# Kernel tuning notes

Hardware: AMD Instinct MI355X
Metric: run time of the kernel (lower is better)

The kernel has to match this reference:

```python
import jax, jax.numpy as jnp
import numpy as np


def _lstm_layer(x, h0, c0, w_ih, w_hh, b):
    """x: [T,B,I], h0/c0: [B,H], w_ih: [4H,I], w_hh: [4H,H], b: [4H]. PyTorch gate order i,f,g,o."""
    H = h0.shape[-1]
    # Precompute input projection for all timesteps in one big GEMM.
    xg = jnp.einsum('tbi,gi->tbg', x, w_ih) + b  # [T,B,4H]

    def step(carry, xg_t):
        h, c = carry
        g = xg_t + h @ w_hh.T  # [B,4H]
        i, f, gg, o = jnp.split(g, 4, axis=-1)
        c_new = jax.nn.sigmoid(f) * c + jax.nn.sigmoid(i) * jnp.tanh(gg)
        h_new = jax.nn.sigmoid(o) * jnp.tanh(c_new)
        return (h_new, c_new), h_new

    (_, _), hs = jax.lax.scan(step, (h0, c0), xg)
    return hs  # [T,B,H]


def setup_inputs() -> dict:
    key = jax.random.key(0)
    ks = jax.random.split(key, 12)
    T, B, I, H, O, L = 2048, 32, 256, 512, 1024, 2
    s = 1.0 / np.sqrt(H)  # PyTorch LSTM init scale
    return {
        'x': jax.random.normal(ks[0], (T, B, I), jnp.float32),
        'h0': jnp.zeros((L, B, H), jnp.float32),
        'c0': jnp.zeros((L, B, H), jnp.float32),
        'w_ih0': jax.random.normal(ks[1], (4 * H, I), jnp.float32) * s,
        'w_hh0': jax.random.normal(ks[2], (4 * H, H), jnp.float32) * s,
        'b_ih0': jax.random.normal(ks[3], (4 * H,), jnp.float32) * s,
        'b_hh0': jax.random.normal(ks[4], (4 * H,), jnp.float32) * s,
        'w_ih1': jax.random.normal(ks[5], (4 * H, H), jnp.float32) * s,
        'w_hh1': jax.random.normal(ks[6], (4 * H, H), jnp.float32) * s,
        'b_ih1': jax.random.normal(ks[7], (4 * H,), jnp.float32) * s,
        'b_hh1': jax.random.normal(ks[8], (4 * H,), jnp.float32) * s,
        'fc_w': jax.random.normal(ks[9], (O, H), jnp.float32) * s,
        'fc_b': jax.random.normal(ks[10], (O,), jnp.float32) * s,
    }


def reference(x, h0, c0, w_ih0, w_hh0, b_ih0, b_hh0, w_ih1, w_hh1, b_ih1, b_hh1, fc_w, fc_b):
    h1 = _lstm_layer(x, h0[0], c0[0], w_ih0, w_hh0, b_ih0 + b_hh0)   # [T,B,H]
    h2 = _lstm_layer(h1, h0[1], c0[1], w_ih1, w_hh1, b_ih1 + b_hh1)  # [T,B,H]
    logits = h2[-1] @ fc_w.T + fc_b  # out[-1] -> fc, [B,O]
    return jax.nn.log_softmax(logits, axis=1)
```

## Files before the change

### kernel.cpp

```cpp
#include <hip/hip_runtime.h>
#include <stdint.h>

#define TT 2048
#define BB 32
#define II 256
#define HH 512
#define OO 1024
#define NWGL 64
#define NWG 128
#define RING 32
#define SLOTB (BB * HH * 2)

typedef __attribute__((ext_vector_type(8))) short short8;
typedef __attribute__((ext_vector_type(4))) float floatx4;

__device__ __forceinline__ unsigned short f2bf(float f) {
  union { float f; unsigned u; } v; v.f = f;
  unsigned r = v.u + 0x7FFFu + ((v.u >> 16) & 1u);
  return (unsigned short)(r >> 16);
}
__device__ __forceinline__ float bf2f(unsigned short b) {
  union { float f; unsigned u; } v; v.u = ((unsigned)b) << 16; return v.f;
}
__device__ __forceinline__ float sigmf(float x) { return 1.0f / (1.0f + __expf(-x)); }
__device__ __forceinline__ float tanhfast(float x) {
  float xc = fminf(fmaxf(x, -15.f), 15.f);
  float e = __expf(2.f * xc);
  return (e - 1.f) / (e + 1.f);
}

#define LD1(d, va, IMM)                                                     \
  asm volatile("global_load_dwordx4 %0, %1, off offset:" IMM " sc0 sc1"     \
               : "=v"(d) : "v"(va) : "memory")
#define LD1C(d, va, IMM)                                                    \
  asm volatile("global_load_dwordx4 %0, %1, off offset:" IMM                \
               : "=v"(d) : "v"(va) : "memory")

#define ISSUE8(dst, va) do {                                                \
    LD1(dst[0], va, "0");   LD1(dst[1], va, "64");                          \
    LD1(dst[2], va, "128"); LD1(dst[3], va, "192");                         \
    LD1(dst[4], va, "256"); LD1(dst[5], va, "320");                         \
    LD1(dst[6], va, "384"); LD1(dst[7], va, "448"); } while (0)
#define ISSUE8C(dst, va) do {                                               \
    LD1C(dst[0], va, "0");   LD1C(dst[1], va, "64");                        \
    LD1C(dst[2], va, "128"); LD1C(dst[3], va, "192");                       \
    LD1C(dst[4], va, "256"); LD1C(dst[5], va, "320");                       \
    LD1C(dst[6], va, "384"); LD1C(dst[7], va, "448"); } while (0)

#define WAITV(N) do {                                                       \
    asm volatile("s_waitcnt vmcnt(" #N ")" ::: "memory");                   \
    __builtin_amdgcn_sched_barrier(0); } while (0)

#define MF8(tt_, src, wbase) do {                                           \
    _Pragma("unroll")                                                       \
    for (int j = 0; j < 8; j++) {                                           \
      acc[0][tt_] = __builtin_amdgcn_mfma_f32_16x16x32_bf16(src[j], wf[0][(wbase) + j], acc[0][tt_], 0, 0, 0); \
      acc[1][tt_] = __builtin_amdgcn_mfma_f32_16x16x32_bf16(src[j], wf[1][(wbase) + j], acc[1][tt_], 0, 0, 0); \
    } } while (0)

#define PROGREAD(dst, addr64)                                               \
  asm volatile("global_load_dword %0, %1, off sc0 sc1"                      \
               : "=v"(dst) : "v"(addr64) : "memory")

#define SEQSTORE(arr, slot, val) do {                                       \
    if (lane == 0) {                                                        \
      unsigned long long _a = (unsigned long long)(arr) +                   \
          (unsigned long long)((slot) * 64 + g) * 4;                        \
      int _v = (val);                                                       \
      asm volatile("global_store_dword %0, %1, off sc0 sc1"                 \
                   :: "v"(_a), "v"(_v) : "memory");                         \
    } } while (0)

#define TAIL(hwaddr) do {                                                   \
  _Pragma("unroll")                                                         \
  for (int tau = 0; tau < 2; tau++) {                                       \
    _Pragma("unroll")                                                       \
    for (int tt = 0; tt < 2; tt++) {                                        \
      _Pragma("unroll")                                                     \
      for (int r = 0; r < 4; r++) {                                         \
        float val = acc[tau][tt][r];                                        \
        float nl = (gate == 2) ? tanhfast(val) : sigmf(val);                \
        int base2 = (lane & 48) | u;                                        \
        float iv = __shfl(nl, base2);                                       \
        float fv = __shfl(nl, base2 | 4);                                   \
        float gv = __shfl(nl, base2 | 8);                                   \
        float ov = __shfl(nl, base2 | 12);                                  \
        if (gate == 0) {                                                    \
          float cn = fv * cst[tau][tt][r] + iv * gv;                        \
          cst[tau][tt][r] = cn;                                             \
          float hn = ov * tanhfast(cn);                                     \
          int b = tt * 16 + krow * 4 + r;                                   \
          sh[b][tau * 4 + u] = f2bf(hn);                                    \
        }                                                                   \
      }                                                                     \
    }                                                                       \
  }                                                                         \
  asm volatile("s_waitcnt lgkmcnt(0)" ::: "memory");                        \
  __builtin_amdgcn_sched_barrier(0);                                        \
  if (lane < 32) {                                                          \
    short8 v = *reinterpret_cast<const short8*>(&sh[lane][0]);              \
    unsigned long long sa = (hwaddr) + stoff;                               \
    asm volatile("global_store_dwordx4 %0, %1, off sc0 sc1"                 \
                 :: "v"(sa), "v"(v) : "memory");                            \
  } } while (0)

__global__ void k_convert_x(const float* __restrict__ x, ushort* __restrict__ xb, int n4) {
  int i = blockIdx.x * blockDim.x + threadIdx.x;
  int stride = gridDim.x * blockDim.x;
  const float4* xf = reinterpret_cast<const float4*>(x);
  ushort4* ob = reinterpret_cast<ushort4*>(xb);
  for (; i < n4; i += stride) {
    float4 f = xf[i];
    ushort4 o;
    o.x = f2bf(f.x); o.y = f2bf(f.y); o.z = f2bf(f.z); o.w = f2bf(f.w);
    ob[i] = o;
  }
}

__global__ void k_init(const float* __restrict__ h0in,
                       ushort* __restrict__ h0ring, ushort* __restrict__ h1ring,
                       int* __restrict__ h0seq, int* __restrict__ h1seq,
                       int* __restrict__ pr1) {
  int i = threadIdx.x;
  ushort* s0 = h0ring + (RING - 1) * BB * HH;
  ushort* s1 = h1ring + (RING - 1) * BB * HH;
  for (int k = i; k < BB * HH; k += blockDim.x) {
    s0[k] = f2bf(h0in[k]);
    s1[k] = f2bf(h0in[BB * HH + k]);
  }
  for (int k = i; k < RING * 64; k += blockDim.x) {
    int v = (k >= (RING - 1) * 64) ? -1 : (int)0x80000000;
    h0seq[k] = v;
    h1seq[k] = v;
  }
  for (int k = i; k < 64; k += blockDim.x) pr1[k] = -1;
}

__global__ __launch_bounds__(64, 1) void k_lstm(
    const ushort* __restrict__ xb,
    const float* __restrict__ w_ih0, const float* __restrict__ w_hh0,
    const float* __restrict__ b_ih0, const float* __restrict__ b_hh0,
    const float* __restrict__ w_ih1, const float* __restrict__ w_hh1,
    const float* __restrict__ b_ih1, const float* __restrict__ b_hh1,
    const float* __restrict__ c0in,
    ushort* __restrict__ h0ring, ushort* __restrict__ h1ring,
    int* __restrict__ h0seq, int* __restrict__ h1seq,
    int* __restrict__ pr1)
{
  __shared__ ushort sh[BB][8];
  const int wg = blockIdx.x;
  const int lane = threadIdx.x;
  const bool isL0 = wg < NWGL;
  const int g = isL0 ? wg : wg - NWGL;
  const int col = lane & 15;
  const int krow = lane >> 4;
  const int u = col & 3;
  const int gate = col >> 2;

  short8 wf[2][32];
#define LOADW(dst, base, rowlen, kbase, tau) do {                             \
    const int _grow = gate * HH + g * 8 + (tau) * 4 + u;                      \
    const float* _p = (base) + (size_t)_grow * (rowlen) + (kbase) + krow * 8; \
    short8 _r;                                                                \
    _Pragma("unroll")                                                         \
    for (int _j = 0; _j < 8; _j++) _r[_j] = (short)f2bf(_p[_j]);              \
    (dst) = _r; } while (0)

  if (isL0) {
#pragma unroll
    for (int tau = 0; tau < 2; tau++) {
#pragma unroll
      for (int kk = 0; kk < 8; kk++)  LOADW(wf[tau][kk],      w_ih0, II, kk * 32, tau);
#pragma unroll
      for (int kk = 0; kk < 16; kk++) LOADW(wf[tau][8 + kk],  w_hh0, HH, kk * 32, tau);
    }
  } else {
#pragma unroll
    for (int tau = 0; tau < 2; tau++) {
#pragma unroll
      for (int kk = 0; kk < 16; kk++) LOADW(wf[tau][kk],      w_ih1, HH, kk * 32, tau);
#pragma unroll
      for (int kk = 0; kk < 16; kk++) LOADW(wf[tau][16 + kk], w_hh1, HH, kk * 32, tau);
    }
  }
  float bias[2];
#pragma unroll
  for (int tau = 0; tau < 2; tau++) {
    const int grow = gate * HH + g * 8 + tau * 4 + u;
    bias[tau] = isL0 ? (b_ih0[grow] + b_hh0[grow]) : (b_ih1[grow] + b_hh1[grow]);
  }

  float cst[2][2][4];
  {
    const float* cbase = c0in + (isL0 ? 0 : 1) * BB * HH;
#pragma unroll
    for (int tau = 0; tau < 2; tau++)
#pragma unroll
      for (int tt = 0; tt < 2; tt++)
#pragma unroll
        for (int r = 0; r < 4; r++) {
          int b = tt * 16 + krow * 4 + r;
          cst[tau][tt][r] = cbase[b * HH + g * 8 + tau * 4 + u];
        }
  }

  const unsigned long long h0rb = (unsigned long long)h0ring;
  const unsigned long long h1rb = (unsigned long long)h1ring;
  const int vo00 = col * 1024 + krow * 16;
  const unsigned long long stoff = (unsigned long long)(lane * 1024 + g * 16);

  short8 wa[8], wb[8], wc[8], wd[8];
  floatx4 acc[2][2];
  const floatx4 bi0 = (floatx4){ bias[0], bias[0], bias[0], bias[0] };
  const floatx4 bi1 = (floatx4){ bias[1], bias[1], bias[1], bias[1] };

  if (isL0) {
    const unsigned long long xbase = (unsigned long long)xb + (col * 512 + krow * 16);
    for (int t = 0; t < TT; ++t) {
      {
        const unsigned long long sa = (unsigned long long)h0seq +
            (unsigned long long)(((t + 31) & 31) * 64 + lane) * 4;
        int sv; PROGREAD(sv, sa); WAITV(0);
        while (!__all(sv == t - 1)) {
          __builtin_amdgcn_s_sleep(1); PROGREAD(sv, sa); WAITV(0);
        }
      }
      if (((t & 7) == 0) && t >= 32) {
        const unsigned long long pa = (unsigned long long)pr1 + lane * 4ull;
        int pv; PROGREAD(pv, pa); WAITV(0);
        while (!__all(pv >= t - 24)) {
          __builtin_amdgcn_s_sleep(4); PROGREAD(pv, pa); WAITV(0);
        }
      }
      acc[0][0] = bi0; acc[0][1] = bi0; acc[1][0] = bi1; acc[1][1] = bi1;
      const unsigned long long ha = h0rb + (unsigned long long)((t + 31) & 31) * SLOTB + vo00;
      const unsigned long long xa = xbase + (unsigned long long)t * (BB * II * 2);
      ISSUE8(wa, ha); ISSUE8(wb, ha + 512); ISSUE8(wc, ha + 16384); ISSUE8(wd, ha + 16896);
      WAITV(24); MF8(0, wa, 8);  ISSUE8C(wa, xa);
      WAITV(24); MF8(0, wb, 16); ISSUE8C(wb, xa + 8192);
      WAITV(24); MF8(1, wc, 8);
      WAITV(16); MF8(1, wd, 16);
      WAITV(8);  MF8(0, wa, 0);
      WAITV(0);  MF8(1, wb, 0);
      TAIL(h0rb + (unsigned long long)(t & 31) * SLOTB);
      WAITV(0);
      SEQSTORE(h0seq, (t & 31), t);
    }
  } else {
    for (int t = 0; t < TT; ++t) {
      {
        const unsigned long long sa0 = (unsigned long long)h0seq +
            (unsigned long long)((t & 31) * 64 + lane) * 4;
        const unsigned long long sa1 = (unsigned long long)h1seq +
            (unsigned long long)(((t + 31) & 31) * 64 + lane) * 4;
        int s0, s1; PROGREAD(s0, sa0); PROGREAD(s1, sa1); WAITV(0);
        while (!(__all(s0 == t) & __all(s1 == t - 1))) {
          __builtin_amdgcn_s_sleep(1);
          PROGREAD(s0, sa0); PROGREAD(s1, sa1); WAITV(0);
        }
      }
      acc[0][0] = bi0; acc[0][1] = bi0; acc[1][0] = bi1; acc[1][1] = bi1;
      const unsigned long long a0 = h0rb + (unsigned long long)(t & 31) * SLOTB + vo00;
      const unsigned long long a1 = h1rb + (unsigned long long)((t + 31) & 31) * SLOTB + vo00;
      ISSUE8(wa, a0); ISSUE8(wb, a0 + 512); ISSUE8(wc, a0 + 16384); ISSUE8(wd, a0 + 16896);
      WAITV(24); MF8(0, wa, 0); ISSUE8(wa, a1);
      WAITV(24); MF8(0, wb, 8); ISSUE8(wb, a1 + 512);
      WAITV(24); MF8(1, wc, 0); ISSUE8(wc, a1 + 16384);
      WAITV(24); MF8(1, wd, 8); ISSUE8(wd, a1 + 16896);
      WAITV(24); MF8(0, wa, 16);
      WAITV(16); MF8(0, wb, 24);
      WAITV(8);  MF8(1, wc, 16);
      WAITV(0);  MF8(1, wd, 24);
      if (lane == 0) {
        unsigned long long pa = (unsigned long long)pr1 + (unsigned long long)g * 4;
        int pv = t;
        asm volatile("global_store_dword %0, %1, off sc0 sc1"
                     :: "v"(pa), "v"(pv) : "memory");
      }
      TAIL(h1rb + (unsigned long long)(t & 31) * SLOTB);
      WAITV(0);
      SEQSTORE(h1seq, (t & 31), t);
    }
  }
}

__global__ __launch_bounds__(256) void k_fc(const ushort* __restrict__ h1,
                                            const float* __restrict__ fcw,
                                            const float* __restrict__ fcb,
                                            float* __restrict__ out) {
  __shared__ float hsh[HH];
  __shared__ float red[256];
  const int b = blockIdx.x, tid = threadIdx.x;
  for (int k = tid; k < HH; k += 256) hsh[k] = bf2f(h1[b * HH + k]);
  __syncthreads();
  float lg[4];
#pragma unroll
  for (int q = 0; q < 4; q++) {
    int o = q * 256 + tid;
    float acc = fcb[o];
    const float* wr = fcw + (size_t)o * HH;
#pragma unroll 4
    for (int k = 0; k < HH; k += 4) {
      float4 w4 = *reinterpret_cast<const float4*>(wr + k);
      acc += hsh[k] * w4.x + hsh[k + 1] * w4.y + hsh[k + 2] * w4.z + hsh[k + 3] * w4.w;
    }
    lg[q] = acc;
  }
  float m = fmaxf(fmaxf(lg[0], lg[1]), fmaxf(lg[2], lg[3]));
  red[tid] = m; __syncthreads();
  for (int s = 128; s > 0; s >>= 1) { if (tid < s) red[tid] = fmaxf(red[tid], red[tid + s]); __syncthreads(); }
  m = red[0]; __syncthreads();
  float se = 0.f;
#pragma unroll
  for (int q = 0; q < 4; q++) se += __expf(lg[q] - m);
  red[tid] = se; __syncthreads();
  for (int s = 128; s > 0; s >>= 1) { if (tid < s) red[tid] += red[tid + s]; __syncthreads(); }
  float lse = m + logf(red[0]);
#pragma unroll
  for (int q = 0; q < 4; q++) out[b * OO + q * 256 + tid] = lg[q] - lse;
}

extern "C" void kernel_launch(void* const* d_in, const int* in_sizes, int n_in,
                              void* d_out, int out_size, void* d_ws, size_t ws_size,
                              hipStream_t stream) {
  const float* x     = (const float*)d_in[0];
  const float* h0    = (const float*)d_in[1];
  const float* c0    = (const float*)d_in[2];
  const float* w_ih0 = (const float*)d_in[3];
  const float* w_hh0 = (const float*)d_in[4];
  const float* b_ih0 = (const float*)d_in[5];
  const float* b_hh0 = (const float*)d_in[6];
  const float* w_ih1 = (const float*)d_in[7];
  const float* w_hh1 = (const float*)d_in[8];
  const float* b_ih1 = (const float*)d_in[9];
  const float* b_hh1 = (const float*)d_in[10];
  const float* fcw   = (const float*)d_in[11];
  const float* fcb   = (const float*)d_in[12];
  float* out = (float*)d_out;

  char* ws = (char*)d_ws;
  size_t off = 0;
  ushort* xb     = (ushort*)(ws + off); off += (size_t)TT * BB * II * 2;
  ushort* h0ring = (ushort*)(ws + off); off += (size_t)RING * BB * HH * 2;
  ushort* h1ring = (ushort*)(ws + off); off += (size_t)RING * BB * HH * 2;
  int* h0seq = (int*)(ws + off); off += RING * 64 * sizeof(int);
  int* h1seq = (int*)(ws + off); off += RING * 64 * sizeof(int);
  int* pr1   = (int*)(ws + off); off += 64 * sizeof(int);

  k_convert_x<<<2048, 256, 0, stream>>>(x, xb, TT * BB * II / 4);
  k_init<<<1, 256, 0, stream>>>(h0, h0ring, h1ring, h0seq, h1seq, pr1);
  k_lstm<<<NWG, 64, 0, stream>>>(xb, w_ih0, w_hh0, b_ih0, b_hh0,
                                 w_ih1, w_hh1, b_ih1, b_hh1, c0,
                                 h0ring, h1ring, h0seq, h1seq, pr1);
  k_fc<<<BB, 256, 0, stream>>>(h1ring + (RING - 1) * BB * HH, fcw, fcb, out);
}
```

Baseline: 16.87 ms.

## Pack four waves per workgroup and share hidden-state tiles through LDS

Each workgroup now holds four wavefronts instead of one, so there are 32 persistent workgroups instead of 128. Within a workgroup the four waves load the previous hidden state cooperatively into swizzled LDS tiles and then each wave reads its MFMA A operands from LDS. Previously every wave fetched the full hidden state from global memory on its own. Only wave 0 polls the sequence flags, and block barriers order the staging. This cuts global traffic and the number of pollers, but adds two __syncthreads per step on the serial recurrence path and reads x directly with plain loads, which no longer overlap with the h loads.

```diff
diff --git a/kernel.cpp b/kernel.cpp
--- a/kernel.cpp
+++ b/kernel.cpp
@@ -6,8 +6,8 @@
 #define II 256
 #define HH 512
 #define OO 1024
-#define NWGL 64
-#define NWG 128
+#define NWGL 16
+#define NWG 32
 #define RING 32
 #define SLOTB (BB * HH * 2)
 
@@ -32,31 +32,26 @@
 #define LD1(d, va, IMM)                                                     \
   asm volatile("global_load_dwordx4 %0, %1, off offset:" IMM " sc0 sc1"     \
                : "=v"(d) : "v"(va) : "memory")
-#define LD1C(d, va, IMM)                                                    \
-  asm volatile("global_load_dwordx4 %0, %1, off offset:" IMM                \
-               : "=v"(d) : "v"(va) : "memory")
-
-#define ISSUE8(dst, va) do {                                                \
-    LD1(dst[0], va, "0");   LD1(dst[1], va, "64");                          \
-    LD1(dst[2], va, "128"); LD1(dst[3], va, "192");                         \
-    LD1(dst[4], va, "256"); LD1(dst[5], va, "320");                         \
-    LD1(dst[6], va, "384"); LD1(dst[7], va, "448"); } while (0)
-#define ISSUE8C(dst, va) do {                                               \
-    LD1C(dst[0], va, "0");   LD1C(dst[1], va, "64");                        \
-    LD1C(dst[2], va, "128"); LD1C(dst[3], va, "192");                       \
-    LD1C(dst[4], va, "256"); LD1C(dst[5], va, "320");                       \
-    LD1C(dst[6], va, "384"); LD1C(dst[7], va, "448"); } while (0)
+
+#define ISSUE8KB(dst, va) do {                                              \
+    unsigned long long _v1 = (va), _v2 = (va) + 4096;                       \
+    LD1(dst[0], _v1, "0");    LD1(dst[1], _v1, "1024");                     \
+    LD1(dst[2], _v1, "2048"); LD1(dst[3], _v1, "3072");                     \
+    LD1(dst[4], _v2, "0");    LD1(dst[5], _v2, "1024");                     \
+    LD1(dst[6], _v2, "2048"); LD1(dst[7], _v2, "3072"); } while (0)
 
 #define WAITV(N) do {                                                       \
     asm volatile("s_waitcnt vmcnt(" #N ")" ::: "memory");                   \
     __builtin_amdgcn_sched_barrier(0); } while (0)
 
-#define MF8(tt_, src, wbase) do {                                           \
+#define DSW8(buf, tile, w8) do {                                            \
     _Pragma("unroll")                                                       \
-    for (int j = 0; j < 8; j++) {                                           \
-      acc[0][tt_] = __builtin_amdgcn_mfma_f32_16x16x32_bf16(src[j], wf[0][(wbase) + j], acc[0][tt_], 0, 0, 0); \
-      acc[1][tt_] = __builtin_amdgcn_mfma_f32_16x16x32_bf16(src[j], wf[1][(wbase) + j], acc[1][tt_], 0, 0, 0); \
-    } } while (0)
+    for (int j = 0; j < 8; j++)                                             \
+      *reinterpret_cast<short8*>(&(tile)[((w8) + j) * 512 + (lane ^ j) * 8]) = (buf)[j]; \
+    } while (0)
+
+#define LDSA(tile, b, kk)                                                   \
+  (*reinterpret_cast<const short8*>(&(tile)[(b) * 512 + (((kk) * 4 + krow) ^ c7) * 8]))
 
 #define PROGREAD(dst, addr64)                                               \
   asm volatile("global_load_dword %0, %1, off sc0 sc1"                      \
@@ -69,6 +64,14 @@
       int _v = (val);                                                       \
       asm volatile("global_store_dword %0, %1, off sc0 sc1"                 \
                    :: "v"(_a), "v"(_v) : "memory");                         \
+    } } while (0)
+
+#define VALIDATE(arr, slot, tag) do {                                       \
+    const unsigned long long _sa = (unsigned long long)(arr) +              \
+        (unsigned long long)((slot) * 64 + lane) * 4;                       \
+    int _sv; PROGREAD(_sv, _sa); WAITV(0);                                  \
+    while (!__all(_sv == (tag))) {                                          \
+      __builtin_amdgcn_s_sleep(1); PROGREAD(_sv, _sa); WAITV(0);            \
     } } while (0)
 
 #define TAIL(hwaddr) do {                                                   \
@@ -90,7 +93,7 @@
           cst[tau][tt][r] = cn;                                             \
           float hn = ov * tanhfast(cn);                                     \
           int b = tt * 16 + krow * 4 + r;                                   \
-          sh[b][tau * 4 + u] = f2bf(hn);                                    \
+          sh[w][b][tau * 4 + u] = f2bf(hn);                                 \
         }                                                                   \
       }                                                                     \
     }                                                                       \
@@ -98,7 +101,7 @@
   asm volatile("s_waitcnt lgkmcnt(0)" ::: "memory");                        \
   __builtin_amdgcn_sched_barrier(0);                                        \
   if (lane < 32) {                                                          \
-    short8 v = *reinterpret_cast<const short8*>(&sh[lane][0]);              \
+    short8 v = *reinterpret_cast<const short8*>(&sh[w][lane][0]);           \
     unsigned long long sa = (hwaddr) + stoff;                               \
     asm volatile("global_store_dwordx4 %0, %1, off sc0 sc1"                 \
                  :: "v"(sa), "v"(v) : "memory");                            \
@@ -136,7 +139,7 @@
   for (int k = i; k < 64; k += blockDim.x) pr1[k] = -1;
 }
 
-__global__ __launch_bounds__(64, 1) void k_lstm(
+__global__ __launch_bounds__(256, 1) void k_lstm(
     const ushort* __restrict__ xb,
     const float* __restrict__ w_ih0, const float* __restrict__ w_hh0,
     const float* __restrict__ b_ih0, const float* __restrict__ b_hh0,
@@ -147,15 +150,21 @@
     int* __restrict__ h0seq, int* __restrict__ h1seq,
     int* __restrict__ pr1)
 {
-  __shared__ ushort sh[BB][8];
+  __shared__ ushort t0[32 * 512];
+  __shared__ ushort t1[32 * 512];
+  __shared__ ushort sh[4][BB][8];
   const int wg = blockIdx.x;
-  const int lane = threadIdx.x;
+  const int tid = threadIdx.x;
+  const int w = tid >> 6;
+  const int lane = tid & 63;
   const bool isL0 = wg < NWGL;
-  const int g = isL0 ? wg : wg - NWGL;
+  const int G = isL0 ? wg : wg - NWGL;
+  const int g = G * 4 + w;
   const int col = lane & 15;
   const int krow = lane >> 4;
   const int u = col & 3;
   const int gate = col >> 2;
+  const int c7 = col & 7;
 
   short8 wf[2][32];
 #define LOADW(dst, base, rowlen, kbase, tau) do {                             \
@@ -206,49 +215,56 @@
 
   const unsigned long long h0rb = (unsigned long long)h0ring;
   const unsigned long long h1rb = (unsigned long long)h1ring;
-  const int vo00 = col * 1024 + krow * 16;
   const unsigned long long stoff = (unsigned long long)(lane * 1024 + g * 16);
-
-  short8 wa[8], wb[8], wc[8], wd[8];
+  const unsigned long long stagevo = (unsigned long long)(w * 8192 + lane * 16);
+
+  short8 wa[8], wb[8];
   floatx4 acc[2][2];
   const floatx4 bi0 = (floatx4){ bias[0], bias[0], bias[0], bias[0] };
   const floatx4 bi1 = (floatx4){ bias[1], bias[1], bias[1], bias[1] };
 
   if (isL0) {
-    const unsigned long long xbase = (unsigned long long)xb + (col * 512 + krow * 16);
     for (int t = 0; t < TT; ++t) {
-      {
-        const unsigned long long sa = (unsigned long long)h0seq +
-            (unsigned long long)(((t + 31) & 31) * 64 + lane) * 4;
-        int sv; PROGREAD(sv, sa); WAITV(0);
-        while (!__all(sv == t - 1)) {
-          __builtin_amdgcn_s_sleep(1); PROGREAD(sv, sa); WAITV(0);
-        }
-      }
-      if (((t & 7) == 0) && t >= 32) {
-        const unsigned long long pa = (unsigned long long)pr1 + lane * 4ull;
-        int pv; PROGREAD(pv, pa); WAITV(0);
-        while (!__all(pv >= t - 24)) {
-          __builtin_amdgcn_s_sleep(4); PROGREAD(pv, pa); WAITV(0);
-        }
-      }
+      if (w == 0) {
+        VALIDATE(h0seq, (t + 31) & 31, t - 1);
+        if (((t & 7) == 0) && t >= 32) {
+          const unsigned long long pa = (unsigned long long)pr1 + lane * 4ull;
+          int pv; PROGREAD(pv, pa); WAITV(0);
+          while (!__all(pv >= t - 24)) {
+            __builtin_amdgcn_s_sleep(4); PROGREAD(pv, pa); WAITV(0);
+          }
+        }
+      }
+      __syncthreads();
+      ISSUE8KB(wa, h0rb + (unsigned long long)((t + 31) & 31) * SLOTB + stagevo);
+      WAITV(0);
+      DSW8(wa, t0, w * 8);
+      __syncthreads();
       acc[0][0] = bi0; acc[0][1] = bi0; acc[1][0] = bi1; acc[1][1] = bi1;
-      const unsigned long long ha = h0rb + (unsigned long long)((t + 31) & 31) * SLOTB + vo00;
-      const unsigned long long xa = xbase + (unsigned long long)t * (BB * II * 2);
-      ISSUE8(wa, ha); ISSUE8(wb, ha + 512); ISSUE8(wc, ha + 16384); ISSUE8(wd, ha + 16896);
-      WAITV(24); MF8(0, wa, 8);  ISSUE8C(wa, xa);
-      WAITV(24); MF8(0, wb, 16); ISSUE8C(wb, xa + 8192);
-      WAITV(24); MF8(1, wc, 8);
-      WAITV(16); MF8(1, wd, 16);
-      WAITV(8);  MF8(0, wa, 0);
-      WAITV(0);  MF8(1, wb, 0);
+      const char* xr = (const char*)xb + (size_t)t * (BB * II * 2);
+#pragma unroll
+      for (int tt = 0; tt < 2; tt++) {
+        const int b = tt * 16 + col;
+#pragma unroll
+        for (int kk = 0; kk < 8; kk++) {
+          short8 a = *reinterpret_cast<const short8*>(xr + b * 512 + kk * 64 + krow * 16);
+          acc[0][tt] = __builtin_amdgcn_mfma_f32_16x16x32_bf16(a, wf[0][kk], acc[0][tt], 0, 0, 0);
+          acc[1][tt] = __builtin_amdgcn_mfma_f32_16x16x32_bf16(a, wf[1][kk], acc[1][tt], 0, 0, 0);
+        }
+#pragma unroll
+        for (int kk = 0; kk < 16; kk++) {
+          short8 a = LDSA(t0, b, kk);
+          acc[0][tt] = __builtin_amdgcn_mfma_f32_16x16x32_bf16(a, wf[0][8 + kk], acc[0][tt], 0, 0, 0);
+          acc[1][tt] = __builtin_amdgcn_mfma_f32_16x16x32_bf16(a, wf[1][8 + kk], acc[1][tt], 0, 0, 0);
+        }
+      }
       TAIL(h0rb + (unsigned long long)(t & 31) * SLOTB);
       WAITV(0);
       SEQSTORE(h0seq, (t & 31), t);
     }
   } else {
     for (int t = 0; t < TT; ++t) {
-      {
+      if (w == 0) {
         const unsigned long long sa0 = (unsigned long long)h0seq +
             (unsigned long long)((t & 31) * 64 + lane) * 4;
         const unsigned long long sa1 = (unsigned long long)h1seq +
@@ -259,23 +275,36 @@
           PROGREAD(s0, sa0); PROGREAD(s1, sa1); WAITV(0);
         }
       }
-      acc[0][0] = bi0; acc[0][1] = bi0; acc[1][0] = bi1; acc[1][1] = bi1;
-      const unsigned long long a0 = h0rb + (unsigned long long)(t & 31) * SLOTB + vo00;
-      const unsigned long long a1 = h1rb + (unsigned long long)((t + 31) & 31) * SLOTB + vo00;
-      ISSUE8(wa, a0); ISSUE8(wb, a0 + 512); ISSUE8(wc, a0 + 16384); ISSUE8(wd, a0 + 16896);
-      WAITV(24); MF8(0, wa, 0); ISSUE8(wa, a1);
-      WAITV(24); MF8(0, wb, 8); ISSUE8(wb, a1 + 512);
-      WAITV(24); MF8(1, wc, 0); ISSUE8(wc, a1 + 16384);
-      WAITV(24); MF8(1, wd, 8); ISSUE8(wd, a1 + 16896);
-      WAITV(24); MF8(0, wa, 16);
-      WAITV(16); MF8(0, wb, 24);
-      WAITV(8);  MF8(1, wc, 16);
-      WAITV(0);  MF8(1, wd, 24);
+      __syncthreads();
+      ISSUE8KB(wa, h0rb + (unsigned long long)(t & 31) * SLOTB + stagevo);
+      ISSUE8KB(wb, h1rb + (unsigned long long)((t + 31) & 31) * SLOTB + stagevo);
+      WAITV(8);
+      DSW8(wa, t0, w * 8);
+      WAITV(0);
+      DSW8(wb, t1, w * 8);
       if (lane == 0) {
         unsigned long long pa = (unsigned long long)pr1 + (unsigned long long)g * 4;
         int pv = t;
         asm volatile("global_store_dword %0, %1, off sc0 sc1"
                      :: "v"(pa), "v"(pv) : "memory");
+      }
+      __syncthreads();
+      acc[0][0] = bi0; acc[0][1] = bi0; acc[1][0] = bi1; acc[1][1] = bi1;
+#pragma unroll
+      for (int tt = 0; tt < 2; tt++) {
+        const int b = tt * 16 + col;
+#pragma unroll
+        for (int kk = 0; kk < 16; kk++) {
+          short8 a = LDSA(t0, b, kk);
+          acc[0][tt] = __builtin_amdgcn_mfma_f32_16x16x32_bf16(a, wf[0][kk], acc[0][tt], 0, 0, 0);
+          acc[1][tt] = __builtin_amdgcn_mfma_f32_16x16x32_bf16(a, wf[1][kk], acc[1][tt], 0, 0, 0);
+        }
+#pragma unroll
+        for (int kk = 0; kk < 16; kk++) {
+          short8 a = LDSA(t1, b, kk);
+          acc[0][tt] = __builtin_amdgcn_mfma_f32_16x16x32_bf16(a, wf[0][16 + kk], acc[0][tt], 0, 0, 0);
+          acc[1][tt] = __builtin_amdgcn_mfma_f32_16x16x32_bf16(a, wf[1][16 + kk], acc[1][tt], 0, 0, 0);
+        }
       }
       TAIL(h1rb + (unsigned long long)(t & 31) * SLOTB);
       WAITV(0);
@@ -349,8 +378,8 @@
 
   k_convert_x<<<2048, 256, 0, stream>>>(x, xb, TT * BB * II / 4);
   k_init<<<1, 256, 0, stream>>>(h0, h0ring, h1ring, h0seq, h1seq, pr1);
-  k_lstm<<<NWG, 64, 0, stream>>>(xb, w_ih0, w_hh0, b_ih0, b_hh0,
-                                 w_ih1, w_hh1, b_ih1, b_hh1, c0,
-                                 h0ring, h1ring, h0seq, h1seq, pr1);
+  k_lstm<<<NWG, 256, 0, stream>>>(xb, w_ih0, w_hh0, b_ih0, b_hh0,
+                                  w_ih1, w_hh1, b_ih1, b_hh1, c0,
+                                  h0ring, h1ring, h0seq, h1seq, pr1);
   k_fc<<<BB, 256, 0, stream>>>(h1ring + (RING - 1) * BB * HH, fcw, fcb, out);
 }
```

Result: slower. 18.02 ms (+6.8%).
